# Kernel optimization log

Measured on AMD Instinct MI355X. Metric: run time of the kernel, lower is better.

## Reference

```python
import jax, jax.numpy as jnp
import numpy as np

ENS, S_DIM, A_DIM, R_DIM, HID, LAYER_NUM = 7, 30, 8, 1, 200, 5
N_HID_LAYERS = LAYER_NUM - 2  # hidden->hidden Linear+Swish blocks


def swish(x):
    return x * jax.nn.sigmoid(x)


def setup_inputs() -> dict:
    key = jax.random.key(0)
    ks = jax.random.split(key, 14)
    N = 32768
    out_dim = S_DIM + R_DIM
    s = jax.random.normal(ks[0], (N, ENS, S_DIM), dtype=jnp.float32)
    a = jax.random.normal(ks[1], (N, ENS, A_DIM), dtype=jnp.float32)
    sc = 0.05
    W1 = jax.random.normal(ks[2], (ENS, S_DIM + A_DIM, HID), dtype=jnp.float32) * sc
    b1 = jax.random.normal(ks[3], (ENS, HID), dtype=jnp.float32) * sc
    Wh = jax.random.normal(ks[4], (N_HID_LAYERS, ENS, HID, HID), dtype=jnp.float32) * sc
    bh = jax.random.normal(ks[5], (N_HID_LAYERS, ENS, HID), dtype=jnp.float32) * sc
    Wmu = jax.random.normal(ks[6], (ENS, HID, out_dim), dtype=jnp.float32) * sc
    bmu = jax.random.normal(ks[7], (ENS, out_dim), dtype=jnp.float32) * sc
    Wsig = jax.random.normal(ks[8], (ENS, HID, out_dim), dtype=jnp.float32) * sc
    bsig = jax.random.normal(ks[9], (ENS, out_dim), dtype=jnp.float32) * sc
    max_lv_s = jnp.ones((1, S_DIM), dtype=jnp.float32) / 2.0
    min_lv_s = jnp.ones((1, S_DIM), dtype=jnp.float32) * -10.0
    max_lv_r = jnp.ones((1, R_DIM), dtype=jnp.float32) / 2.0
    min_lv_r = jnp.ones((1, R_DIM), dtype=jnp.float32) * -10.0
    return {"s": s, "a": a, "W1": W1, "b1": b1, "Wh": Wh, "bh": bh,
            "Wmu": Wmu, "bmu": bmu, "Wsig": Wsig, "bsig": bsig,
            "max_lv_s": max_lv_s, "min_lv_s": min_lv_s,
            "max_lv_r": max_lv_r, "min_lv_r": min_lv_r}


def reference(s, a, W1, b1, Wh, bh, Wmu, bmu, Wsig, bsig,
              max_lv_s, min_lv_s, max_lv_r, min_lv_r):
    # x: [N, E, s+a]; per-ensemble-member weights batched along E
    x = jnp.concatenate([s, a], axis=-1)
    h = swish(jnp.einsum('ned,edh->neh', x, W1) + b1)
    for i in range(Wh.shape[0]):
        h = swish(jnp.einsum('neh,ehk->nek', h, Wh[i]) + bh[i])
    mu = jnp.einsum('neh,eho->neo', h, Wmu) + bmu      # [N, E, s+r]
    sigma = jnp.einsum('neh,eho->neo', h, Wsig) + bsig  # raw logvar/2
    ds_mu, r_mu = mu[..., :S_DIM], mu[..., S_DIM:]
    ds_sg, r_sg = sigma[..., :S_DIM], sigma[..., S_DIM:]
    # soft clamping of log-variance, then exp
    ds_sg = (max_lv_s - jax.nn.softplus(max_lv_s - 2.0 * ds_sg)) / 2.0
    ds_sg = (min_lv_s + jax.nn.softplus(2.0 * ds_sg - min_lv_s)) / 2.0
    ds_sg = jnp.exp(ds_sg)
    r_sg = (max_lv_r - jax.nn.softplus(max_lv_r - 2.0 * r_sg)) / 2.0
    r_sg = (min_lv_r + jax.nn.softplus(2.0 * r_sg - min_lv_r)) / 2.0
    r_sg = jnp.exp(r_sg)
    return ((ds_mu, ds_sg), (r_mu, r_sg))
```

## Files before the change

### kernel.cpp

```cpp
#include <hip/hip_runtime.h>
#include <hip/hip_bf16.h>

#define ENS 7
#define SDIM 30
#define ADIM 8
#define DIN 38
#define HID 200
#define DOUT 31
#define NHL 3
#define HS 232
#define MT 32

typedef __bf16 bf16x8 __attribute__((ext_vector_type(8)));
typedef float f32x4 __attribute__((ext_vector_type(4)));

#define U_L1 13312
#define U_H 46592
#define OFF_HD2 (U_L1 + NHL * U_H)
#define PER_E (OFF_HD2 + 14336)
#define WS_TOTAL (ENS * PER_E)

__device__ __forceinline__ unsigned short f2bf(float f) {
    unsigned u = __float_as_uint(f);
    u += 0x7fffu + ((u >> 16) & 1u);
    return (unsigned short)(u >> 16);
}

__device__ __forceinline__ unsigned pk2(float a, float b) {
    __hip_bfloat162 h = __float22bfloat162_rn(make_float2(a, b));
    return *reinterpret_cast<unsigned*>(&h);
}

__device__ __forceinline__ float softplusf(float x) {
    return fmaxf(x, 0.f) + __logf(1.f + __expf(-fabsf(x)));
}

__global__ void prep_kernel(const float* __restrict__ W1, const float* __restrict__ Wh,
                            const float* __restrict__ Wmu, const float* __restrict__ Wsig,
                            unsigned short* __restrict__ ws) {
    int idx = blockIdx.x * 256 + threadIdx.x;
    if (idx >= WS_TOTAL) return;
    int e = idx / PER_E, r = idx % PER_E;
    int j = r & 7, lane = (r >> 3) & 63;
    int l16 = lane & 15, q = lane >> 4;
    float v = 0.f;
    if (r < U_L1) {
        int fi = r >> 9;
        int ct = fi >> 1, st = fi & 1;
        int k = st * 32 + q * 8 + j, n = ct * 16 + l16;
        if (k < DIN && n < HID) v = W1[(e * DIN + k) * HID + n];
    } else if (r < OFF_HD2) {
        int rh = r - U_L1;
        int l = rh / U_H, r2 = rh % U_H;
        int fi = r2 >> 9;
        int ct = fi / 7, st = fi % 7;
        int k = st * 32 + q * 8 + j, n = ct * 16 + l16;
        if (k < HID && n < HID) v = Wh[((l * ENS + e) * HID + (long)k) * HID + n];
    } else {
        int r2 = r - OFF_HD2;
        int fi = r2 >> 9;
        int ct = fi / 7, st = fi % 7;
        int k = st * 32 + q * 8 + j, n = ct * 16 + l16;
        if (k < HID) {
            if (n < DOUT) v = Wmu[(e * HID + k) * DOUT + n];
            else if (n >= 32 && n < 32 + DOUT) v = Wsig[(e * HID + k) * DOUT + (n - 32)];
        }
    }
    ws[idx] = f2bf(v);
}

template<int S, int OWN>
__device__ __forceinline__ void runLayer(const unsigned short* __restrict__ fo,
                                         const unsigned short* __restrict__ fs,
                                         const unsigned short* hA,
                                         int lo, bool sh, int swv, int l16, int quad,
                                         f32x4 (&accO)[2][3], f32x4& accS) {
#pragma unroll
    for (int r = 0; r < 2; r++)
#pragma unroll
        for (int c = 0; c < 3; c++) accO[r][c] = (f32x4){0.f, 0.f, 0.f, 0.f};
    accS = (f32x4){0.f, 0.f, 0.f, 0.f};

#pragma unroll
    for (int st = 0; st < S; ++st) {
        bf16x8 bq[4];
#pragma unroll
        for (int c = 0; c < OWN; c++) bq[c] = *((const bf16x8*)(fo + (c * S + st) * 512 + lo));
        if (sh) bq[3] = *((const bf16x8*)(fs + st * 512 + lo));
        bf16x8 af[2];
#pragma unroll
        for (int r = 0; r < 2; r++)
            af[r] = *((const bf16x8*)(hA + (r * 16 + l16) * HS + st * 32 + quad * 8));
        bf16x8 afs;
        if (sh) afs = *((const bf16x8*)(hA + (swv * 16 + l16) * HS + st * 32 + quad * 8));
#pragma unroll
        for (int c = 0; c < OWN; c++)
#pragma unroll
            for (int r = 0; r < 2; r++)
                accO[r][c] = __builtin_amdgcn_mfma_f32_16x16x32_bf16(bq[c], af[r], accO[r][c], 0, 0, 0);
        if (sh) accS = __builtin_amdgcn_mfma_f32_16x16x32_bf16(bq[3], afs, accS, 0, 0, 0);
    }
}

__launch_bounds__(256, 4)
__global__ void ens_mlp_kernel(const float* __restrict__ s, const float* __restrict__ a,
                               const float* __restrict__ b1, const float* __restrict__ bh,
                               const float* __restrict__ bmu, const float* __restrict__ bsig,
                               const float* __restrict__ maxs, const float* __restrict__ mins,
                               const float* __restrict__ maxr, const float* __restrict__ minr,
                               const unsigned short* __restrict__ ws,
                               float* __restrict__ out, int N) {
    __shared__ unsigned short hA[MT * HS];

    const int tid = threadIdx.x;
    const int wv = tid >> 6, lane = tid & 63;
    const int quad = lane >> 4, l16 = lane & 15;
    const int swv = __builtin_amdgcn_readfirstlane(wv);
    const bool sh = (swv < 2);
    const int lo = lane * 8;
    const int bid = blockIdx.x;
    const int e = bid % ENS, n0 = (bid / ENS) * MT;

    for (int i = tid; i < MT * HS / 8; i += 256) ((uint4*)hA)[i] = make_uint4(0, 0, 0, 0);
    __syncthreads();

    {
        int m = tid & 31, cg = tid >> 5;
        long g = n0 + m;
        const float* srow = s + (g * ENS + e) * SDIM;
        const float* arow = a + (g * ENS + e) * ADIM;
#pragma unroll
        for (int k = 0; k < 5; k++) {
            int c = cg * 5 + k;
            if (c < DIN) {
                float v = (c < SDIM) ? srow[c] : arow[c - SDIM];
                hA[m * HS + c] = f2bf(v);
            }
        }
    }
    __syncthreads();

    const unsigned short* we = ws + e * PER_E;
    const unsigned short* L1o = we + swv * 3 * 2 * 512;
    const unsigned short* L1s = we + 12 * 2 * 512;
    const unsigned short* H0o = we + U_L1 + swv * 3 * 7 * 512;
    const unsigned short* H0s = we + U_L1 + 12 * 7 * 512;
    const unsigned short* H1o = H0o + U_H;
    const unsigned short* H1s = H0s + U_H;
    const unsigned short* H2o = H1o + U_H;
    const unsigned short* H2s = H1s + U_H;
    const unsigned short* HDo = we + OFF_HD2 + swv * 7 * 512;

    f32x4 accO[2][3];
    f32x4 accS;

    auto epiH = [&](const float* bias) {
#pragma unroll
        for (int c = 0; c < 3; c++) {
            int col = (3 * swv + c) * 16 + quad * 4;
            float4 bc4 = *((const float4*)(bias + col));
#pragma unroll
            for (int r = 0; r < 2; r++) {
                float v0 = accO[r][c][0] + bc4.x, v1 = accO[r][c][1] + bc4.y;
                float v2 = accO[r][c][2] + bc4.z, v3 = accO[r][c][3] + bc4.w;
                v0 *= __builtin_amdgcn_rcpf(1.f + __expf(-v0));
                v1 *= __builtin_amdgcn_rcpf(1.f + __expf(-v1));
                v2 *= __builtin_amdgcn_rcpf(1.f + __expf(-v2));
                v3 *= __builtin_amdgcn_rcpf(1.f + __expf(-v3));
                *((uint2*)(hA + (r * 16 + l16) * HS + col)) = make_uint2(pk2(v0, v1), pk2(v2, v3));
            }
        }
        if (sh) {
            int col = 192 + quad * 4;
            float4 bc4 = make_float4(0.f, 0.f, 0.f, 0.f);
            if (col < HID) bc4 = *((const float4*)(bias + col));
            float v0 = accS[0] + bc4.x, v1 = accS[1] + bc4.y;
            float v2 = accS[2] + bc4.z, v3 = accS[3] + bc4.w;
            v0 *= __builtin_amdgcn_rcpf(1.f + __expf(-v0));
            v1 *= __builtin_amdgcn_rcpf(1.f + __expf(-v1));
            v2 *= __builtin_amdgcn_rcpf(1.f + __expf(-v2));
            v3 *= __builtin_amdgcn_rcpf(1.f + __expf(-v3));
            *((uint2*)(hA + (swv * 16 + l16) * HS + col)) = make_uint2(pk2(v0, v1), pk2(v2, v3));
        }
    };

    runLayer<2, 3>(L1o, L1s, hA, lo, sh, swv, l16, quad, accO, accS);
    __syncthreads();
    epiH(b1 + e * HID);
    __syncthreads();
    runLayer<7, 3>(H0o, H0s, hA, lo, sh, swv, l16, quad, accO, accS);
    __syncthreads();
    epiH(bh + (0 * ENS + e) * HID);
    __syncthreads();
    runLayer<7, 3>(H1o, H1s, hA, lo, sh, swv, l16, quad, accO, accS);
    __syncthreads();
    epiH(bh + (1 * ENS + e) * HID);
    __syncthreads();
    runLayer<7, 3>(H2o, H2s, hA, lo, sh, swv, l16, quad, accO, accS);
    __syncthreads();
    epiH(bh + (2 * ENS + e) * HID);
    __syncthreads();
    runLayer<7, 1>(HDo, (const unsigned short*)nullptr,
                   hA, lo, false, swv, l16, quad, accO, accS);

    const long off1 = (long)N * ENS * SDIM;
    const long off2 = 2 * off1;
    const long off3 = off2 + (long)N * ENS;
    {
        const bool isSig = (swv >= 2);
        const int c0 = (swv & 1) * 16 + quad * 4;
        float bias_i[4], mx_i[4], mn_i[4];
#pragma unroll
        for (int i = 0; i < 4; i++) {
            int c = c0 + i;
            bias_i[i] = (c < DOUT) ? (isSig ? bsig : bmu)[e * DOUT + c] : 0.f;
            if (isSig) {
                mx_i[i] = (c < SDIM) ? maxs[c] : maxr[0];
                mn_i[i] = (c < SDIM) ? mins[c] : minr[0];
            }
        }
#pragma unroll
        for (int r = 0; r < 2; r++) {
            long g = n0 + r * 16 + l16;
            long rowbase = (g * ENS + e) * SDIM;
#pragma unroll
            for (int i = 0; i < 4; i++) {
                int c = c0 + i;
                if (c < DOUT) {
                    float v = accO[r][0][i] + bias_i[i];
                    if (!isSig) {
                        if (c < SDIM) out[rowbase + c] = v;
                        else out[off2 + g * ENS + e] = v;
                    } else {
                        v = 0.5f * (mx_i[i] - softplusf(mx_i[i] - 2.f * v));
                        v = 0.5f * (mn_i[i] + softplusf(2.f * v - mn_i[i]));
                        v = __expf(v);
                        if (c < SDIM) out[off1 + rowbase + c] = v;
                        else out[off3 + g * ENS + e] = v;
                    }
                }
            }
        }
    }
}

extern "C" void kernel_launch(void* const* d_in, const int* in_sizes, int n_in,
                              void* d_out, int out_size, void* d_ws, size_t ws_size,
                              hipStream_t stream) {
    const float* s    = (const float*)d_in[0];
    const float* a    = (const float*)d_in[1];
    const float* W1   = (const float*)d_in[2];
    const float* b1   = (const float*)d_in[3];
    const float* Wh   = (const float*)d_in[4];
    const float* bh   = (const float*)d_in[5];
    const float* Wmu  = (const float*)d_in[6];
    const float* bmu  = (const float*)d_in[7];
    const float* Wsig = (const float*)d_in[8];
    const float* bsig = (const float*)d_in[9];
    const float* maxs = (const float*)d_in[10];
    const float* mins = (const float*)d_in[11];
    const float* maxr = (const float*)d_in[12];
    const float* minr = (const float*)d_in[13];
    float* out = (float*)d_out;
    unsigned short* ws = (unsigned short*)d_ws;

    int N = in_sizes[0] / (ENS * SDIM);

    int prepBlocks = (WS_TOTAL + 255) / 256;
    prep_kernel<<<prepBlocks, 256, 0, stream>>>(W1, Wh, Wmu, Wsig, ws);

    int mainBlocks = (N / MT) * ENS;
    ens_mlp_kernel<<<mainBlocks, 256, 0, stream>>>(s, a, b1, bh, bmu, bsig,
                                                   maxs, mins, maxr, minr, ws, out, N);
}
```

Measured before the change: 251.6 us.

## Prefetch next-step weight fragments across layers and reorder blocks by ensemble

Software-pipelines the weight fragment loads in each layer loop. The next k-step's B fragments, or the first step of the following layer, are loaded into registers while the current MFMAs run, which hides global/L2 latency across layer boundaries. Block indexing now groups blocks by ensemble member (e-major) so that concurrent blocks share weights in cache. Zeroing of the hA tile is limited to the padding regions and the initial barrier is dropped. The extra live bf16x8 registers may increase register pressure at launch bounds of 4 blocks.

```diff
diff --git a/kernel.cpp b/kernel.cpp
--- a/kernel.cpp
+++ b/kernel.cpp
@@ -69,12 +69,14 @@
     ws[idx] = f2bf(v);
 }
 
-template<int S, int OWN>
+template<int S, int OWN, int NS, int NOWN, bool NSH>
 __device__ __forceinline__ void runLayer(const unsigned short* __restrict__ fo,
                                          const unsigned short* __restrict__ fs,
+                                         const unsigned short* __restrict__ nfo,
+                                         const unsigned short* __restrict__ nfs,
                                          const unsigned short* hA,
                                          int lo, bool sh, int swv, int l16, int quad,
-                                         f32x4 (&accO)[2][3], f32x4& accS) {
+                                         f32x4 (&accO)[2][3], f32x4& accS, bf16x8 (&bq)[4]) {
 #pragma unroll
     for (int r = 0; r < 2; r++)
 #pragma unroll
@@ -83,10 +85,16 @@
 
 #pragma unroll
     for (int st = 0; st < S; ++st) {
-        bf16x8 bq[4];
-#pragma unroll
-        for (int c = 0; c < OWN; c++) bq[c] = *((const bf16x8*)(fo + (c * S + st) * 512 + lo));
-        if (sh) bq[3] = *((const bf16x8*)(fs + st * 512 + lo));
+        bf16x8 bn[4];
+        if (st + 1 < S) {
+#pragma unroll
+            for (int c = 0; c < OWN; c++) bn[c] = *((const bf16x8*)(fo + (c * S + st + 1) * 512 + lo));
+            if (sh) bn[3] = *((const bf16x8*)(fs + (st + 1) * 512 + lo));
+        } else if (NS > 0) {
+#pragma unroll
+            for (int c = 0; c < NOWN; c++) bn[c] = *((const bf16x8*)(nfo + (c * NS) * 512 + lo));
+            if (NSH && sh) bn[3] = *((const bf16x8*)(nfs + lo));
+        }
         bf16x8 af[2];
 #pragma unroll
         for (int r = 0; r < 2; r++)
@@ -99,6 +107,10 @@
             for (int r = 0; r < 2; r++)
                 accO[r][c] = __builtin_amdgcn_mfma_f32_16x16x32_bf16(bq[c], af[r], accO[r][c], 0, 0, 0);
         if (sh) accS = __builtin_amdgcn_mfma_f32_16x16x32_bf16(bq[3], afs, accS, 0, 0, 0);
+        if (st + 1 < S || NS > 0) {
+#pragma unroll
+            for (int c = 0; c < 4; c++) bq[c] = bn[c];
+        }
     }
 }
 
@@ -119,10 +131,17 @@
     const bool sh = (swv < 2);
     const int lo = lane * 8;
     const int bid = blockIdx.x;
-    const int e = bid % ENS, n0 = (bid / ENS) * MT;
-
-    for (int i = tid; i < MT * HS / 8; i += 256) ((uint4*)hA)[i] = make_uint4(0, 0, 0, 0);
-    __syncthreads();
+    const int bpe = (int)((unsigned)N / MT);
+    const int e = bid / bpe, n0 = (bid % bpe) * MT;
+
+    for (int t = tid; t < 32 * 13; t += 256) {
+        int row = t / 13, k = t % 13;
+        *((unsigned*)(hA + row * HS + 38 + 2 * k)) = 0u;
+    }
+    for (int t = tid; t < 32 * 12; t += 256) {
+        int row = t / 12, k = t % 12;
+        *((unsigned*)(hA + row * HS + 208 + 2 * k)) = 0u;
+    }
 
     {
         int m = tid & 31, cg = tid >> 5;
@@ -153,6 +172,7 @@
 
     f32x4 accO[2][3];
     f32x4 accS;
+    bf16x8 bq[4];
 
     auto epiH = [&](const float* bias) {
 #pragma unroll
@@ -184,24 +204,30 @@
         }
     };
 
-    runLayer<2, 3>(L1o, L1s, hA, lo, sh, swv, l16, quad, accO, accS);
+#pragma unroll
+    for (int c = 0; c < 3; c++) bq[c] = *((const bf16x8*)(L1o + (c * 2) * 512 + lo));
+    if (sh) bq[3] = *((const bf16x8*)(L1s + lo));
+
+    runLayer<2, 3, 7, 3, true>(L1o, L1s, H0o, H0s, hA, lo, sh, swv, l16, quad, accO, accS, bq);
     __syncthreads();
     epiH(b1 + e * HID);
     __syncthreads();
-    runLayer<7, 3>(H0o, H0s, hA, lo, sh, swv, l16, quad, accO, accS);
+    runLayer<7, 3, 7, 3, true>(H0o, H0s, H1o, H1s, hA, lo, sh, swv, l16, quad, accO, accS, bq);
     __syncthreads();
     epiH(bh + (0 * ENS + e) * HID);
     __syncthreads();
-    runLayer<7, 3>(H1o, H1s, hA, lo, sh, swv, l16, quad, accO, accS);
+    runLayer<7, 3, 7, 3, true>(H1o, H1s, H2o, H2s, hA, lo, sh, swv, l16, quad, accO, accS, bq);
     __syncthreads();
     epiH(bh + (1 * ENS + e) * HID);
     __syncthreads();
-    runLayer<7, 3>(H2o, H2s, hA, lo, sh, swv, l16, quad, accO, accS);
+    runLayer<7, 3, 7, 1, false>(H2o, H2s, HDo, (const unsigned short*)nullptr,
+                                hA, lo, sh, swv, l16, quad, accO, accS, bq);
     __syncthreads();
     epiH(bh + (2 * ENS + e) * HID);
     __syncthreads();
-    runLayer<7, 1>(HDo, (const unsigned short*)nullptr,
-                   hA, lo, false, swv, l16, quad, accO, accS);
+    runLayer<7, 1, 0, 0, false>(HDo, (const unsigned short*)nullptr,
+                                (const unsigned short*)nullptr, (const unsigned short*)nullptr,
+                                hA, lo, false, swv, l16, quad, accO, accS, bq);
 
     const long off1 = (long)N * ENS * SDIM;
     const long off2 = 2 * off1;
```

Result: slower. 262.6 us (+4.4%).
